# Kernel optimization log

Hardware: AMD Instinct MI355X
Metric: run time of the kernel (lower is better)

The kernel has to match this reference:

```python
import jax, jax.numpy as jnp
import numpy as np

# Fixed B3-spline 5-tap weights (non-trainable in the torch module)
W5 = jnp.array([1/16, 1/4, 3/8, 1/4, 1/16], dtype=jnp.float32)
LEVEL = 3  # J
DIM = 2    # spatial dims (H, W)


def _conv1d_reflect(y, axis, dil):
    """5-tap dilated conv along `axis` with reflect padding of 2*dil (same size).

    Matches torch Conv1d(1,1,5, dilation=dil, padding=2*dil, padding_mode='reflect').
    """
    p = 2 * dil
    pads = [(0, 0)] * y.ndim
    pads[axis] = (p, p)
    yp = jnp.pad(y, pads, mode='reflect')  # torch 'reflect' == jnp 'reflect'
    L = y.shape[axis]
    out = W5[0] * jax.lax.slice_in_dim(yp, 0, L, axis=axis)
    for k in range(1, 5):
        out = out + W5[k] * jax.lax.slice_in_dim(yp, k * dil, k * dil + L, axis=axis)
    return out


def setup_inputs() -> dict:
    key = jax.random.key(0)
    x = jax.random.normal(key, (16, 1024, 1024), dtype=jnp.float32)  # (B, H, W)
    return {"x": x}


def reference(x):
    # x: (B, H, W); returns (B, LEVEL+1, H, W) = [w_1, ..., w_J, c_J]
    y = x
    details = []
    for j in range(LEVEL):
        prev = y
        dil = 2 ** j
        for axis in range(1, 1 + DIM):  # spatial axes of (B, H, W)
            y = _conv1d_reflect(y, axis, dil)
        details.append(prev - y)  # w_{j+1}
    return jnp.stack(details + [y], axis=1)
```

## Files before the change

### kernel.cpp

```cpp
#include <hip/hip_runtime.h>


#define HH 1024
#define WW 1024
#define TXT 64
#define TYT 32
#define BY 60
#define BXS 104
#define NC8 12

typedef unsigned short u16;
typedef unsigned int u32;

__device__ __forceinline__ int reflect_i(int g, int n) {
    if (g < 0) g = -g;
    else if (g >= n) g = 2 * n - 2 - g;
    return g;
}

__device__ __forceinline__ float bl(u32 u) { return __uint_as_float(u << 16); }
__device__ __forceinline__ float bh(u32 u) { return __uint_as_float(u & 0xffff0000u); }

__device__ __forceinline__ u32 pack2(float a, float b) {
    u32 ua = __float_as_uint(a); ua += 0x7fff + ((ua >> 16) & 1);
    u32 ub = __float_as_uint(b); ub += 0x7fff + ((ub >> 16) & 1);
    return (ua >> 16) | (ub & 0xffff0000u);
}

__device__ __forceinline__ void unpack8(uint4 v, float* f) {
    f[0] = bl(v.x); f[1] = bh(v.x);
    f[2] = bl(v.y); f[3] = bh(v.y);
    f[4] = bl(v.z); f[5] = bh(v.z);
    f[6] = bl(v.w); f[7] = bh(v.w);
}

__device__ constexpr float K0 = 1.0f / 16.0f;
__device__ constexpr float K1 = 4.0f / 16.0f;
__device__ constexpr float K2 = 6.0f / 16.0f;

template <int D, int H0, int NRB>
__device__ __forceinline__ void vpass(const u16* S, u16* Dst, int tid) {
    constexpr int CNT = NRB * NC8;
    for (int u = tid; u < CNT; u += 256) {
        int rb = u / NC8, c8 = u - rb * NC8;
        int base = H0 + (rb % D) + (rb / D) * (4 * D);
        const u16* sp = S + 8 * c8;
        uint4 rv[8];
#pragma unroll
        for (int j = 0; j < 8; ++j)
            rv[j] = *(const uint4*)(sp + (base + (j - 2) * D) * BXS);
        uint4 ov[4];
#pragma unroll
        for (int p = 0; p < 4; ++p) {
            u32 rp[8];
#pragma unroll
            for (int j = 0; j < 8; ++j) rp[j] = ((const u32*)&rv[j])[p];
#pragma unroll
            for (int t = 0; t < 4; ++t) {
                float lo = K0 * (bl(rp[t]) + bl(rp[t + 4])) + K1 * (bl(rp[t + 1]) + bl(rp[t + 3])) + K2 * bl(rp[t + 2]);
                float hi = K0 * (bh(rp[t]) + bh(rp[t + 4])) + K1 * (bh(rp[t + 1]) + bh(rp[t + 3])) + K2 * bh(rp[t + 2]);
                ((u32*)&ov[t])[p] = pack2(lo, hi);
            }
        }
        u16* dp = Dst + 8 * c8;
#pragma unroll
        for (int t = 0; t < 4; ++t)
            *(uint4*)(dp + (base + t * D) * BXS) = ov[t];
    }
}

template <int D, int H0, int NR, int C8LO, int NC, int LVL>
__device__ __forceinline__ void hpass(u16* A, const u16* Bs, float* __restrict__ out,
                                      int tx0, int ty0, int bz, int tid) {
    constexpr int CNT = NR * NC;
    for (int u = tid; u < CNT; u += 256) {
        int ri = u / NC, ci = u - ri * NC;
        int c8 = C8LO + ci, r = H0 + ri;
        const u16* br = Bs + r * BXS;
        int cm = (c8 > 0 ? c8 - 1 : 0);
        int cp = (c8 < NC8 - 1 ? c8 + 1 : NC8 - 1);
        float v[24];
        unpack8(*(const uint4*)(br + 8 * cm), v);
        unpack8(*(const uint4*)(br + 8 * c8), v + 8);
        unpack8(*(const uint4*)(br + 8 * cp), v + 16);
        float o[8];
#pragma unroll
        for (int i = 0; i < 8; ++i)
            o[i] = K0 * (v[8 + i - 2 * D] + v[8 + i + 2 * D]) + K1 * (v[8 + i - D] + v[8 + i + D]) + K2 * v[8 + i];
        u16* ap = A + r * BXS + 8 * c8;
        float old[8];
        unpack8(*(const uint4*)ap, old);
        uint4 nv;
        nv.x = pack2(o[0], o[1]); nv.y = pack2(o[2], o[3]);
        nv.z = pack2(o[4], o[5]); nv.w = pack2(o[6], o[7]);
        *(uint4*)ap = nv;
        bool st = (LVL == 2) || (r >= 14 && r < 46 && c8 >= 2 && c8 < 10);
        if (st) {
            int h = ty0 + r - 14, w = tx0 + 8 * c8 - 16;
            size_t base = ((((size_t)bz) * 4 + LVL) * HH + h) * (size_t)WW + w;
            *(float4*)(out + base)     = make_float4(old[0] - o[0], old[1] - o[1], old[2] - o[2], old[3] - o[3]);
            *(float4*)(out + base + 4) = make_float4(old[4] - o[4], old[5] - o[5], old[6] - o[6], old[7] - o[7]);
            if (LVL == 2) {
                size_t cbase = base + (size_t)HH * WW;
                *(float4*)(out + cbase)     = make_float4(o[0], o[1], o[2], o[3]);
                *(float4*)(out + cbase + 4) = make_float4(o[4], o[5], o[6], o[7]);
            }
        }
    }
}

__global__ __launch_bounds__(256) void uwt3_bf16(const float* __restrict__ x,
                                                 float* __restrict__ out) {
    __shared__ u16 A[BY * BXS];
    __shared__ u16 Bs[BY * BXS];
    const int tid = threadIdx.x;
    const int tx0 = blockIdx.x * TXT;
    const int ty0 = blockIdx.y * TYT;
    const int bz = blockIdx.z;
    const float* xb = x + (size_t)bz * HH * WW;

    for (int i = tid; i < BY * NC8; i += 256) {
        int r = i / NC8, c8 = i - r * NC8;
        int gr = reflect_i(ty0 + r - 14, HH);
        int w0 = tx0 + 8 * c8 - 16;
        const float* row = xb + (size_t)gr * WW;
        float f[8];
        if (w0 >= 0 && w0 + 7 < WW) {
            float4 a = *(const float4*)(row + w0);
            float4 b = *(const float4*)(row + w0 + 4);
            f[0] = a.x; f[1] = a.y; f[2] = a.z; f[3] = a.w;
            f[4] = b.x; f[5] = b.y; f[6] = b.z; f[7] = b.w;
        } else {
#pragma unroll
            for (int k = 0; k < 8; ++k) f[k] = row[reflect_i(w0 + k, WW)];
        }
        uint4 v;
        v.x = pack2(f[0], f[1]); v.y = pack2(f[2], f[3]);
        v.z = pack2(f[4], f[5]); v.w = pack2(f[6], f[7]);
        *(uint4*)(A + r * BXS + 8 * c8) = v;
    }
    __syncthreads();

    vpass<1, 2, 14>(A, Bs, tid);
    __syncthreads();
    hpass<1, 2, 56, 0, 12, 0>(A, Bs, out, tx0, ty0, bz, tid);
    __syncthreads();

    vpass<2, 6, 12>(A, Bs, tid);
    __syncthreads();
    hpass<2, 6, 48, 1, 10, 1>(A, Bs, out, tx0, ty0, bz, tid);
    __syncthreads();

    vpass<4, 14, 8>(A, Bs, tid);
    __syncthreads();
    hpass<4, 14, 32, 2, 8, 2>(A, Bs, out, tx0, ty0, bz, tid);
}

extern "C" void kernel_launch(void* const* d_in, const int* in_sizes, int n_in,
                              void* d_out, int out_size, void* d_ws, size_t ws_size,
                              hipStream_t stream) {
    const float* x = (const float*)d_in[0];
    float* out = (float*)d_out;
    dim3 grid(WW / TXT, HH / TYT, 16);
    uwt3_bf16<<<grid, dim3(256, 1, 1), 0, stream>>>(x, out);
}
```

Baseline: 351.7 us.

## Rewrite wavelet as row-streaming kernel with ring buffers and shuffle-based horizontal pass

Replaces the tiled kernel, which loaded a full haloed tile and ran separate vertical and horizontal passes per level, with a kernel that streams 8-row chunks down a 224-wide, 64-row stripe. Each level keeps its intermediate rows in a 32-row shared-memory ring, and the horizontal halo is exchanged between lanes with warp shuffles instead of shared-memory reads. All four output planes are written at the end with nontemporal stores. This cuts redundant halo recomputation and shared-memory traffic, at the cost of three barriers per chunk, a pipeline warm-up of four chunks, and partial work in the last stripe column.

Measured after the change: 373.8 us. 6.3% more time.

```diff
diff --git a/kernel.cpp b/kernel.cpp
--- a/kernel.cpp
+++ b/kernel.cpp
@@ -3,157 +3,167 @@
 
 #define HH 1024
 #define WW 1024
-#define TXT 64
-#define TYT 32
-#define BY 60
-#define BXS 104
-#define NC8 12
+#define STRIDE 256
+#define EMITW 224
+#define HSEG 64
+#define NCH (HSEG / 8 + 4)
 
 typedef unsigned short u16;
 typedef unsigned int u32;
+typedef float f4 __attribute__((ext_vector_type(4)));
 
 __device__ __forceinline__ int reflect_i(int g, int n) {
     if (g < 0) g = -g;
     else if (g >= n) g = 2 * n - 2 - g;
     return g;
 }
-
 __device__ __forceinline__ float bl(u32 u) { return __uint_as_float(u << 16); }
 __device__ __forceinline__ float bh(u32 u) { return __uint_as_float(u & 0xffff0000u); }
-
 __device__ __forceinline__ u32 pack2(float a, float b) {
     u32 ua = __float_as_uint(a); ua += 0x7fff + ((ua >> 16) & 1);
     u32 ub = __float_as_uint(b); ub += 0x7fff + ((ub >> 16) & 1);
     return (ua >> 16) | (ub & 0xffff0000u);
 }
-
 __device__ __forceinline__ void unpack8(uint4 v, float* f) {
     f[0] = bl(v.x); f[1] = bh(v.x);
     f[2] = bl(v.y); f[3] = bh(v.y);
     f[4] = bl(v.z); f[5] = bh(v.z);
     f[6] = bl(v.w); f[7] = bh(v.w);
 }
-
 __device__ constexpr float K0 = 1.0f / 16.0f;
 __device__ constexpr float K1 = 4.0f / 16.0f;
 __device__ constexpr float K2 = 6.0f / 16.0f;
 
-template <int D, int H0, int NRB>
-__device__ __forceinline__ void vpass(const u16* S, u16* Dst, int tid) {
-    constexpr int CNT = NRB * NC8;
-    for (int u = tid; u < CNT; u += 256) {
-        int rb = u / NC8, c8 = u - rb * NC8;
-        int base = H0 + (rb % D) + (rb / D) * (4 * D);
-        const u16* sp = S + 8 * c8;
-        uint4 rv[8];
+__device__ __forceinline__ int rslot(int q) { return (q + 128) & 31; }
+
+template <int D>
+__device__ __forceinline__ void conv_vh(const u16* __restrict__ src, int q, int c8,
+                                        int lane, float* h) {
+    uint4 tv[5];
 #pragma unroll
-        for (int j = 0; j < 8; ++j)
-            rv[j] = *(const uint4*)(sp + (base + (j - 2) * D) * BXS);
-        uint4 ov[4];
+    for (int k = 0; k < 5; ++k)
+        tv[k] = *(const uint4*)(src + rslot(q + (k - 2) * D) * STRIDE + 8 * c8);
+    float v8[8];
+    {
+        float a[8], b[8];
+        unpack8(tv[0], a); unpack8(tv[4], b);
 #pragma unroll
-        for (int p = 0; p < 4; ++p) {
-            u32 rp[8];
+        for (int c = 0; c < 8; ++c) v8[c] = K0 * (a[c] + b[c]);
+        unpack8(tv[1], a); unpack8(tv[3], b);
 #pragma unroll
-            for (int j = 0; j < 8; ++j) rp[j] = ((const u32*)&rv[j])[p];
+        for (int c = 0; c < 8; ++c) v8[c] += K1 * (a[c] + b[c]);
+        unpack8(tv[2], a);
 #pragma unroll
-            for (int t = 0; t < 4; ++t) {
-                float lo = K0 * (bl(rp[t]) + bl(rp[t + 4])) + K1 * (bl(rp[t + 1]) + bl(rp[t + 3])) + K2 * bl(rp[t + 2]);
-                float hi = K0 * (bh(rp[t]) + bh(rp[t + 4])) + K1 * (bh(rp[t + 1]) + bh(rp[t + 3])) + K2 * bh(rp[t + 2]);
-                ((u32*)&ov[t])[p] = pack2(lo, hi);
-            }
-        }
-        u16* dp = Dst + 8 * c8;
+        for (int c = 0; c < 8; ++c) v8[c] += K2 * a[c];
+    }
+    float ext[8 + 4 * D];
 #pragma unroll
-        for (int t = 0; t < 4; ++t)
-            *(uint4*)(dp + (base + t * D) * BXS) = ov[t];
+    for (int c = 0; c < 8; ++c) ext[2 * D + c] = v8[c];
+#pragma unroll
+    for (int j = 0; j < 2 * D; ++j) {
+        ext[j]             = __shfl(v8[8 - 2 * D + j], lane - 1);
+        ext[2 * D + 8 + j] = __shfl(v8[j], lane + 1);
     }
+#pragma unroll
+    for (int c = 0; c < 8; ++c)
+        h[c] = K0 * (ext[c] + ext[c + 4 * D]) + K1 * (ext[c + D] + ext[c + 3 * D])
+             + K2 * ext[c + 2 * D];
 }
 
-template <int D, int H0, int NR, int C8LO, int NC, int LVL>
-__device__ __forceinline__ void hpass(u16* A, const u16* Bs, float* __restrict__ out,
-                                      int tx0, int ty0, int bz, int tid) {
-    constexpr int CNT = NR * NC;
-    for (int u = tid; u < CNT; u += 256) {
-        int ri = u / NC, ci = u - ri * NC;
-        int c8 = C8LO + ci, r = H0 + ri;
-        const u16* br = Bs + r * BXS;
-        int cm = (c8 > 0 ? c8 - 1 : 0);
-        int cp = (c8 < NC8 - 1 ? c8 + 1 : NC8 - 1);
-        float v[24];
-        unpack8(*(const uint4*)(br + 8 * cm), v);
-        unpack8(*(const uint4*)(br + 8 * c8), v + 8);
-        unpack8(*(const uint4*)(br + 8 * cp), v + 16);
-        float o[8];
+__device__ __forceinline__ void ring_write(u16* dst, int q, int c8, const float* h) {
+    uint4 ov;
+    ov.x = pack2(h[0], h[1]); ov.y = pack2(h[2], h[3]);
+    ov.z = pack2(h[4], h[5]); ov.w = pack2(h[6], h[7]);
+    *(uint4*)(dst + rslot(q) * STRIDE + 8 * c8) = ov;
+}
+
+__device__ __forceinline__ void nt4(float* p, float a, float b, float c, float d) {
+    f4 v; v.x = a; v.y = b; v.z = c; v.w = d;
+    __builtin_nontemporal_store(v, (f4*)p);
+}
+
+__global__ __launch_bounds__(256, 3) void uwt3_stream(const float* __restrict__ x,
+                                                      float* __restrict__ out) {
+    __shared__ __align__(16) u16 ring[3][32][STRIDE];
+    u16* xr  = &ring[0][0][0];
+    u16* y1r = &ring[1][0][0];
+    u16* y2r = &ring[2][0][0];
+    const int tid = threadIdx.x;
+    const int lane = tid & 63;
+    const int rowic = 2 * (tid >> 6) + (lane >> 5);
+    const int c8 = lane & 31;
+    const int stripe0 = blockIdx.x * EMITW;
+    const int R0 = blockIdx.y * HSEG;
+    const int bz = blockIdx.z;
+    const float* xb = x + (size_t)bz * HH * WW;
+    const size_t PL = (size_t)HH * WW;
+
+    for (int t = 0; t < NCH; ++t) {
+        const int r = R0 - 32 + 8 * t;
+
+        {
+            int q = r + 14 + rowic;
+            int gr = reflect_i(q, HH);
+            int w0 = stripe0 - 16 + 8 * c8;
+            const float* row = xb + (size_t)gr * WW;
+            float f[8];
+            if (w0 >= 0 && w0 + 7 < WW) {
+                float4 a = *(const float4*)(row + w0);
+                float4 b = *(const float4*)(row + w0 + 4);
+                f[0] = a.x; f[1] = a.y; f[2] = a.z; f[3] = a.w;
+                f[4] = b.x; f[5] = b.y; f[6] = b.z; f[7] = b.w;
+            } else {
 #pragma unroll
-        for (int i = 0; i < 8; ++i)
-            o[i] = K0 * (v[8 + i - 2 * D] + v[8 + i + 2 * D]) + K1 * (v[8 + i - D] + v[8 + i + D]) + K2 * v[8 + i];
-        u16* ap = A + r * BXS + 8 * c8;
-        float old[8];
-        unpack8(*(const uint4*)ap, old);
-        uint4 nv;
-        nv.x = pack2(o[0], o[1]); nv.y = pack2(o[2], o[3]);
-        nv.z = pack2(o[4], o[5]); nv.w = pack2(o[6], o[7]);
-        *(uint4*)ap = nv;
-        bool st = (LVL == 2) || (r >= 14 && r < 46 && c8 >= 2 && c8 < 10);
-        if (st) {
-            int h = ty0 + r - 14, w = tx0 + 8 * c8 - 16;
-            size_t base = ((((size_t)bz) * 4 + LVL) * HH + h) * (size_t)WW + w;
-            *(float4*)(out + base)     = make_float4(old[0] - o[0], old[1] - o[1], old[2] - o[2], old[3] - o[3]);
-            *(float4*)(out + base + 4) = make_float4(old[4] - o[4], old[5] - o[5], old[6] - o[6], old[7] - o[7]);
-            if (LVL == 2) {
-                size_t cbase = base + (size_t)HH * WW;
-                *(float4*)(out + cbase)     = make_float4(o[0], o[1], o[2], o[3]);
-                *(float4*)(out + cbase + 4) = make_float4(o[4], o[5], o[6], o[7]);
+                for (int k = 0; k < 8; ++k) f[k] = row[reflect_i(w0 + k, WW)];
+            }
+            uint4 v;
+            v.x = pack2(f[0], f[1]); v.y = pack2(f[2], f[3]);
+            v.z = pack2(f[4], f[5]); v.w = pack2(f[6], f[7]);
+            *(uint4*)(xr + rslot(q) * STRIDE + 8 * c8) = v;
+        }
+        __syncthreads();
+
+        if (t >= 1) {
+            float h[8];
+            int q = r + 12 + rowic;
+            conv_vh<1>(xr, q, c8, lane, h);
+            ring_write(y1r, q, c8, h);
+        }
+        __syncthreads();
+
+        if (t >= 2) {
+            float h[8];
+            int q = r + 8 + rowic;
+            conv_vh<2>(y1r, q, c8, lane, h);
+            ring_write(y2r, q, c8, h);
+        }
+        __syncthreads();
+
+        if (t >= 4) {
+            int q = r + rowic;
+            float h[8];
+            conv_vh<4>(y2r, q, c8, lane, h);
+            if (c8 >= 2 && c8 < 30) {
+                int w = stripe0 + 8 * c8 - 16;
+                if (w < WW) {
+                    float xv[8], a1[8], a2[8];
+                    const int so = rslot(q) * STRIDE + 8 * c8;
+                    unpack8(*(const uint4*)(xr + so), xv);
+                    unpack8(*(const uint4*)(y1r + so), a1);
+                    unpack8(*(const uint4*)(y2r + so), a2);
+                    size_t b0 = (((size_t)bz * 4) * HH + q) * (size_t)WW + w;
+                    nt4(out + b0,              xv[0]-a1[0], xv[1]-a1[1], xv[2]-a1[2], xv[3]-a1[3]);
+                    nt4(out + b0 + 4,          xv[4]-a1[4], xv[5]-a1[5], xv[6]-a1[6], xv[7]-a1[7]);
+                    nt4(out + b0 + PL,         a1[0]-a2[0], a1[1]-a2[1], a1[2]-a2[2], a1[3]-a2[3]);
+                    nt4(out + b0 + PL + 4,     a1[4]-a2[4], a1[5]-a2[5], a1[6]-a2[6], a1[7]-a2[7]);
+                    nt4(out + b0 + 2*PL,       a2[0]-h[0],  a2[1]-h[1],  a2[2]-h[2],  a2[3]-h[3]);
+                    nt4(out + b0 + 2*PL + 4,   a2[4]-h[4],  a2[5]-h[5],  a2[6]-h[6],  a2[7]-h[7]);
+                    nt4(out + b0 + 3*PL,       h[0], h[1], h[2], h[3]);
+                    nt4(out + b0 + 3*PL + 4,   h[4], h[5], h[6], h[7]);
+                }
             }
         }
     }
-}
-
-__global__ __launch_bounds__(256) void uwt3_bf16(const float* __restrict__ x,
-                                                 float* __restrict__ out) {
-    __shared__ u16 A[BY * BXS];
-    __shared__ u16 Bs[BY * BXS];
-    const int tid = threadIdx.x;
-    const int tx0 = blockIdx.x * TXT;
-    const int ty0 = blockIdx.y * TYT;
-    const int bz = blockIdx.z;
-    const float* xb = x + (size_t)bz * HH * WW;
-
-    for (int i = tid; i < BY * NC8; i += 256) {
-        int r = i / NC8, c8 = i - r * NC8;
-        int gr = reflect_i(ty0 + r - 14, HH);
-        int w0 = tx0 + 8 * c8 - 16;
-        const float* row = xb + (size_t)gr * WW;
-        float f[8];
-        if (w0 >= 0 && w0 + 7 < WW) {
-            float4 a = *(const float4*)(row + w0);
-            float4 b = *(const float4*)(row + w0 + 4);
-            f[0] = a.x; f[1] = a.y; f[2] = a.z; f[3] = a.w;
-            f[4] = b.x; f[5] = b.y; f[6] = b.z; f[7] = b.w;
-        } else {
-#pragma unroll
-            for (int k = 0; k < 8; ++k) f[k] = row[reflect_i(w0 + k, WW)];
-        }
-        uint4 v;
-        v.x = pack2(f[0], f[1]); v.y = pack2(f[2], f[3]);
-        v.z = pack2(f[4], f[5]); v.w = pack2(f[6], f[7]);
-        *(uint4*)(A + r * BXS + 8 * c8) = v;
-    }
-    __syncthreads();
-
-    vpass<1, 2, 14>(A, Bs, tid);
-    __syncthreads();
-    hpass<1, 2, 56, 0, 12, 0>(A, Bs, out, tx0, ty0, bz, tid);
-    __syncthreads();
-
-    vpass<2, 6, 12>(A, Bs, tid);
-    __syncthreads();
-    hpass<2, 6, 48, 1, 10, 1>(A, Bs, out, tx0, ty0, bz, tid);
-    __syncthreads();
-
-    vpass<4, 14, 8>(A, Bs, tid);
-    __syncthreads();
-    hpass<4, 14, 32, 2, 8, 2>(A, Bs, out, tx0, ty0, bz, tid);
 }
 
 extern "C" void kernel_launch(void* const* d_in, const int* in_sizes, int n_in,
@@ -161,6 +171,6 @@
                               hipStream_t stream) {
     const float* x = (const float*)d_in[0];
     float* out = (float*)d_out;
-    dim3 grid(WW / TXT, HH / TYT, 16);
-    uwt3_bf16<<<grid, dim3(256, 1, 1), 0, stream>>>(x, out);
+    dim3 grid((WW + EMITW - 1) / EMITW, HH / HSEG, 16);
+    uwt3_stream<<<grid, dim3(256, 1, 1), 0, stream>>>(x, out);
 }
```
